# Kernel optimization log

Hardware: AMD Instinct MI355X
Metric: run time of the kernel (lower is better)

The kernel has to match this reference:

```python
import jax, jax.numpy as jnp
import numpy as np

N_NODES = 50000
EMB = 256
HEADS = 8
NEG_SLOPE = 0.2


def gat_conv(x, src, dst, W, a_src, a_dst, b, num_nodes):
    # x: [N, Din]; W: [Din, H, F]; a_src/a_dst: [H, F]; b: [H*F]
    h = jnp.einsum('nd,dhf->nhf', x, W)                      # [N, H, F]
    al_s = jnp.sum(h * a_src, axis=-1)                       # [N, H]
    al_d = jnp.sum(h * a_dst, axis=-1)                       # [N, H]
    logits = jax.nn.leaky_relu(al_s[src] + al_d[dst], NEG_SLOPE)  # [E, H]
    # segment softmax over incoming edges of each destination node
    m = jax.ops.segment_max(logits, dst, num_segments=num_nodes)  # [N, H]
    e = jnp.exp(logits - m[dst])                              # [E, H]
    z = jax.ops.segment_sum(e, dst, num_segments=num_nodes)   # [N, H]
    alpha = e / (z[dst] + 1e-16)                              # [E, H]
    msg = h[src] * alpha[..., None]                           # [E, H, F]
    out = jax.ops.segment_sum(msg, dst, num_segments=num_nodes)  # [N, H, F]
    return out.reshape(num_nodes, -1) + b


def setup_inputs() -> dict:
    key = jax.random.key(0)
    ks = jax.random.split(key, 10)
    F1 = EMB // HEADS  # 32
    x = jax.random.normal(ks[0], (N_NODES, EMB), dtype=jnp.float32)
    edge_index = jax.random.randint(ks[1], (2, 800000), 0, N_NODES, dtype=jnp.int64)
    s1 = 1.0 / np.sqrt(EMB)
    W1 = jax.random.normal(ks[2], (EMB, HEADS, F1), dtype=jnp.float32) * s1
    a_src1 = jax.random.normal(ks[3], (HEADS, F1), dtype=jnp.float32) * s1
    a_dst1 = jax.random.normal(ks[4], (HEADS, F1), dtype=jnp.float32) * s1
    b1 = jnp.zeros((HEADS * F1,), dtype=jnp.float32)
    W2 = jax.random.normal(ks[5], (EMB, 1, EMB), dtype=jnp.float32) * s1
    a_src2 = jax.random.normal(ks[6], (1, EMB), dtype=jnp.float32) * s1
    a_dst2 = jax.random.normal(ks[7], (1, EMB), dtype=jnp.float32) * s1
    b2 = jnp.zeros((EMB,), dtype=jnp.float32)
    return {"x": x, "edge_index": edge_index,
            "W1": W1, "a_src1": a_src1, "a_dst1": a_dst1, "b1": b1,
            "W2": W2, "a_src2": a_src2, "a_dst2": a_dst2, "b2": b2}


def reference(x, edge_index, W1, a_src1, a_dst1, b1, W2, a_src2, a_dst2, b2):
    n = x.shape[0]
    loops = jnp.arange(n, dtype=edge_index.dtype)
    src = jnp.concatenate([edge_index[0], loops])
    dst = jnp.concatenate([edge_index[1], loops])
    h = gat_conv(x, src, dst, W1, a_src1, a_dst1, b1, n)   # [N, EMB]
    out = gat_conv(h, src, dst, W2, a_src2, a_dst2, b2, n)  # [N, EMB]
    return out
```

## Files before the change

kernel.cpp:

```cpp
#include <hip/hip_runtime.h>
#include <hip/hip_bf16.h>

typedef unsigned short u16;
typedef unsigned int   u32;

typedef __attribute__((ext_vector_type(8))) short s16x8;
typedef __attribute__((ext_vector_type(8))) unsigned short u16x8;
typedef __attribute__((ext_vector_type(4))) float f32x4;

#define CAP 64

__device__ __forceinline__ float b2f(u16 u) {
    union { u32 i; float f; } v; v.i = ((u32)u) << 16; return v.f;
}
__device__ __forceinline__ u16 f2b(float f) {
    union { float f; u32 i; } v; v.f = f;
    u32 u = v.i;
    u32 r = (u + 0x7fffu + ((u >> 16) & 1u)) >> 16;
    return (u16)r;
}

__device__ __forceinline__ int detect_f32(const u16* xw) {
    int t = threadIdx.x & 63;
    u16 w = xw[2 * t];
    int e = (w >> 7) & 0xFF;
    bool sane = (e >= 112 && e <= 131);
    unsigned long long m1 = __ballot(sane);
    return (__popcll(m1) >= 32) ? 0 : 1;
}

__device__ __forceinline__ int edge_at(const int* __restrict__ ei, int i64f, long long j) {
    return i64f ? ei[2 * j] : ei[(size_t)j];
}

__device__ __forceinline__ u16x8 loadA8(const void* __restrict__ A, size_t eoff, int f32f) {
    if (f32f) {
        const float* p = (const float*)A + eoff;
        float4 v0 = *(const float4*)p;
        float4 v1 = *(const float4*)(p + 4);
        u16x8 r;
        r[0] = f2b(v0.x); r[1] = f2b(v0.y); r[2] = f2b(v0.z); r[3] = f2b(v0.w);
        r[4] = f2b(v1.x); r[5] = f2b(v1.y); r[6] = f2b(v1.z); r[7] = f2b(v1.w);
        return r;
    }
    return *(const u16x8*)((const u16*)A + eoff);
}

__global__ __launch_bounds__(256) void prep(const void* __restrict__ x,
                                            const int* __restrict__ ei,
                                            const void* __restrict__ W1, const void* __restrict__ W2,
                                            const void* p0, const void* p1, const void* p2,
                                            const void* p3, const void* p4, const void* p5,
                                            u16* __restrict__ wt1, u16* __restrict__ wt2,
                                            u16* __restrict__ sv,
                                            int* __restrict__ cur, u16* __restrict__ csr,
                                            int* __restrict__ flags, u16* __restrict__ hp,
                                            u16* __restrict__ wsd1t, u16* __restrict__ wsd2t,
                                            int ZB, int CF, int NN) {
    int b = blockIdx.x, t = threadIdx.x;
    int f32f = detect_f32((const u16*)x);
    if (b < 512) {
        const void* W = (b < 256) ? W1 : W2;
        u16* Wt = (b < 256) ? wt1 : wt2;
        int k = b & 255;
        u16 v = f32f ? f2b(((const float*)W)[k * 256 + t]) : ((const u16*)W)[k * 256 + t];
        Wt[t * 256 + k] = v;
        return;
    }
    b -= 512;
    if (b == 0) {
        const void* ps[6] = {p0, p1, p2, p3, p4, p5};
#pragma unroll
        for (int j = 0; j < 6; j++) {
            u16 v = f32f ? f2b(((const float*)ps[j])[t]) : ((const u16*)ps[j])[t];
            sv[j * 256 + t] = v;
        }
        hp[(size_t)NN * 256 + t] = 0;
        {
            int k = t;
            for (int h = 0; h < 8; h++) {
                float s = 0.f, d = 0.f;
                for (int f0 = 0; f0 < 32; f0 += 8) {
                    int idx = h * 32 + f0;
                    u16x8 wv = loadA8(W1, (size_t)k * 256 + idx, f32f);
                    u16x8 av = loadA8(p0, idx, f32f);
                    u16x8 dv = loadA8(p1, idx, f32f);
#pragma unroll
                    for (int j = 0; j < 8; j++) {
                        float w = b2f(wv[j]);
                        s += w * b2f(av[j]);
                        d += w * b2f(dv[j]);
                    }
                }
                wsd1t[h * 256 + k] = f2b(s);
                wsd1t[(8 + h) * 256 + k] = f2b(d);
            }
            float s2 = 0.f, d2 = 0.f;
            for (int f0 = 0; f0 < 256; f0 += 8) {
                u16x8 wv = loadA8(W2, (size_t)k * 256 + f0, f32f);
                u16x8 av = loadA8(p3, f0, f32f);
                u16x8 dv = loadA8(p4, f0, f32f);
#pragma unroll
                for (int j = 0; j < 8; j++) {
                    float w = b2f(wv[j]);
                    s2 += w * b2f(av[j]);
                    d2 += w * b2f(dv[j]);
                }
            }
            for (int cc = 0; cc < 16; cc++) wsd2t[cc * 256 + k] = 0;
            wsd2t[k] = f2b(s2);
            wsd2t[8 * 256 + k] = f2b(d2);
        }
        if (t < 64) {
            bool hz = (ei[2 * t + 1] == 0);
            unsigned long long m2 = __ballot(hz);
            if (t == 0) {
                flags[0] = f32f;
                flags[1] = (m2 == ~0ull) ? 1 : 0;
            }
        }
        return;
    }
    b -= 1;
    if (b < ZB) {
        int i = b * 256 + t;
        if (i < (NN + 3) / 4) ((int4*)cur)[i] = make_int4(0, 0, 0, 0);
        return;
    }
    b -= ZB;
    if (b < CF) {
        int i = b * 256 + t;
        int pat = (NN & 0xFFFF) | (NN << 16);
        if (i < NN * (CAP / 8)) ((int4*)csr)[i] = make_int4(pat, pat, pat, pat);
        return;
    }
}

__global__ __launch_bounds__(256) void gemm_tiled(const void* __restrict__ A,
                                                  const u16* __restrict__ Bt,
                                                  u16* __restrict__ C, int M,
                                                  const int* __restrict__ flags, int dynA,
                                                  const u16* __restrict__ wsdT,
                                                  float* __restrict__ als,
                                                  float* __restrict__ ald, int H,
                                                  const int* __restrict__ ei,
                                                  int* __restrict__ cur,
                                                  u16* __restrict__ csr,
                                                  int E, int ET, int gtA) {
    __shared__ u16 sA[128 * 32];
    __shared__ u16 sB[128 * 32];
    if ((int)blockIdx.x >= gtA) {
        int i = (blockIdx.x - gtA) * 256 + threadIdx.x;
        if (i < ET) {
            int i64f = flags[1];
            int s, d;
            if (i < E) { s = edge_at(ei, i64f, i); d = edge_at(ei, i64f, (long long)E + i); }
            else       { s = d = i - E; }
            int p = atomicAdd(&cur[d], 1);
            if (p < CAP) csr[d * CAP + p] = (u16)s;
        }
        return;
    }
    if (blockIdx.x == 0 && threadIdx.x < (unsigned)H)
        als[(size_t)M * H + threadIdx.x] = -1e30f;

    int f32a = dynA ? flags[0] : 0;
    int tid = threadIdx.x;
    int mt = blockIdx.x >> 1, nt = blockIdx.x & 1;
    int r0 = mt * 128, c0 = nt * 128;
    int w = tid >> 6, lane = tid & 63;
    int wr = w & 1, wc = w >> 1;
    int lm = lane & 15, quad = lane >> 4;
    bool doE = (nt == 0) && (w < 2);

    int row0 = tid >> 2, ch0 = tid & 3;
    int row1 = row0 + 64;
    int ga0 = r0 + row0; if (ga0 >= M) ga0 = M - 1;
    int ga1 = r0 + row1; if (ga1 >= M) ga1 = M - 1;
    size_t aoff0 = (size_t)ga0 * 256 + ch0 * 8;
    size_t aoff1 = (size_t)ga1 * 256 + ch0 * 8;
    const u16* Bb0 = Bt + (size_t)(c0 + row0) * 256 + ch0 * 8;
    const u16* Bb1 = Bt + (size_t)(c0 + row1) * 256 + ch0 * 8;

    u16x8 ra0 = loadA8(A, aoff0, f32a);
    u16x8 ra1 = loadA8(A, aoff1, f32a);
    u16x8 rb0 = *(const u16x8*)Bb0;
    u16x8 rb1 = *(const u16x8*)Bb1;

    f32x4 acc[4][4];
#pragma unroll
    for (int i = 0; i < 4; i++)
#pragma unroll
        for (int j = 0; j < 4; j++) acc[i][j] = (f32x4){0.f, 0.f, 0.f, 0.f};
    f32x4 acc_e[4];
#pragma unroll
    for (int i = 0; i < 4; i++) acc_e[i] = (f32x4){0.f, 0.f, 0.f, 0.f};

    u16* wA0 = sA + row0 * 32 + ch0 * 8;
    u16* wA1 = sA + row1 * 32 + ch0 * 8;
    u16* wB0 = sB + row0 * 32 + ch0 * 8;
    u16* wB1 = sB + row1 * 32 + ch0 * 8;
    const u16* rA = sA + (wr * 64 + lm) * 32 + quad * 8;
    const u16* rB = sB + (wc * 64 + lm) * 32 + quad * 8;

    for (int kb = 0; kb < 8; kb++) {
        __syncthreads();
        *(u16x8*)wA0 = ra0;
        *(u16x8*)wA1 = ra1;
        *(u16x8*)wB0 = rb0;
        *(u16x8*)wB1 = rb1;
        __syncthreads();
        if (kb < 7) {
            int ko = (kb + 1) * 32;
            ra0 = loadA8(A, aoff0 + ko, f32a);
            ra1 = loadA8(A, aoff1 + ko, f32a);
            rb0 = *(const u16x8*)(Bb0 + ko);
            rb1 = *(const u16x8*)(Bb1 + ko);
        }
        s16x8 af[4], bf[4];
#pragma unroll
        for (int fr = 0; fr < 4; fr++) af[fr] = *(const s16x8*)(rA + fr * 16 * 32);
#pragma unroll
        for (int fc = 0; fc < 4; fc++) bf[fc] = *(const s16x8*)(rB + fc * 16 * 32);
#pragma unroll
        for (int fr = 0; fr < 4; fr++)
#pragma unroll
            for (int fc = 0; fc < 4; fc++)
                acc[fr][fc] = __builtin_amdgcn_mfma_f32_16x16x32_bf16(af[fr], bf[fc], acc[fr][fc], 0, 0, 0);
        if (doE) {
            s16x8 bfe = *(const s16x8*)(wsdT + (size_t)lm * 256 + kb * 32 + quad * 8);
#pragma unroll
            for (int fr = 0; fr < 4; fr++)
                acc_e[fr] = __builtin_amdgcn_mfma_f32_16x16x32_bf16(af[fr], bfe, acc_e[fr], 0, 0, 0);
        }
    }

#pragma unroll
    for (int fr = 0; fr < 4; fr++) {
#pragma unroll
        for (int fc = 0; fc < 4; fc++) {
#pragma unroll
            for (int r = 0; r < 4; r++) {
                int row = r0 + wr * 64 + fr * 16 + quad * 4 + r;
                if (row < M) C[(size_t)row * 256 + c0 + wc * 64 + fc * 16 + lm] = f2b(acc[fr][fc][r]);
            }
        }
    }
    if (doE) {
#pragma unroll
        for (int fr = 0; fr < 4; fr++) {
#pragma unroll
            for (int r = 0; r < 4; r++) {
                int row = r0 + wr * 64 + fr * 16 + quad * 4 + r;
                if (row < M) {
                    float v = acc_e[fr][r];
                    if (H == 8) {
                        if (lm < 8) als[(size_t)row * 8 + lm] = v;
                        else        ald[(size_t)row * 8 + (lm - 8)] = v;
                    } else {
                        if (lm == 0)      als[row] = v;
                        else if (lm == 8) ald[row] = v;
                    }
                }
            }
        }
    }
}

template <int H, int FINAL>
__global__ __launch_bounds__(256) void gat_agg(const u16* __restrict__ hsrc,
                                               const float* __restrict__ al_s,
                                               const float* __restrict__ al_d,
                                               const int* __restrict__ degv,
                                               const u16* __restrict__ csr16,
                                               const u16* __restrict__ bias,
                                               u16* __restrict__ out_b16,
                                               void* __restrict__ out_final,
                                               const int* __restrict__ flags, int N) {
    int wid = threadIdx.x >> 6, lane = threadIdx.x & 63;
    int c = lane * 4;
    int hc = (H == 8) ? (lane >> 3) : 0;
    int he = lane & (H - 1);
    int j8 = lane >> 3;
    const u16* hb = hsrc + c;
    ushort4 bv = *(const ushort4*)(bias + c);
    int f32f = FINAL ? flags[0] : 0;
    int step = gridDim.x * 8;

    for (int n0 = blockIdx.x * 8 + wid * 2; n0 < N; n0 += step) {
        int nA = n0, nB = n0 + 1;
        int hasB = (nB < N) ? 1 : 0;
        int degA = degv[nA]; degA = degA < CAP ? degA : CAP;
        int degB = hasB ? degv[nB] : 0; degB = degB < CAP ? degB : CAP;
        int padA = (degA + 7) & ~7;
        int padB = (degB + 7) & ~7;
        const u16* cA = csr16 + nA * CAP;
        const u16* cB = csr16 + nB * CAP;
        float adA = al_d[(size_t)nA * H + he];
        float adB = hasB ? al_d[(size_t)nB * H + he] : 0.f;

        float aA0 = 0.f, aA1 = 0.f, aA2 = 0.f, aA3 = 0.f, zA = 0.f;
        float aB0 = 0.f, aB1 = 0.f, aB2 = 0.f, aB3 = 0.f, zB = 0.f;

        int gmax = padA > padB ? padA : padB;
        for (int g = 0; g < gmax; g += 8) {
            int doA = g < padA, doB = g < padB;
            if (doA & doB) {
                int smA = cA[g + j8];
                int smB = cB[g + j8];
                float vA = al_s[(size_t)smA * H + he] + adA;
                float vB = al_s[(size_t)smB * H + he] + adB;
                vA = vA > 0.f ? vA : 0.2f * vA;
                vB = vB > 0.f ? vB : 0.2f * vB;
                float eA = __expf(vA);
                float eB = __expf(vB);
#pragma unroll
                for (int j = 0; j < 8; j++) {
                    int   sjA = __shfl(smA, j * 8, 64);
                    int   sjB = __shfl(smB, j * 8, 64);
                    float ejA = __shfl(eA, j * 8 + hc, 64);
                    float ejB = __shfl(eB, j * 8 + hc, 64);
                    ushort4 hvA = *(const ushort4*)(hb + (size_t)sjA * 256);
                    ushort4 hvB = *(const ushort4*)(hb + (size_t)sjB * 256);
                    zA += ejA;
                    aA0 += ejA * b2f(hvA.x); aA1 += ejA * b2f(hvA.y);
                    aA2 += ejA * b2f(hvA.z); aA3 += ejA * b2f(hvA.w);
                    zB += ejB;
                    aB0 += ejB * b2f(hvB.x); aB1 += ejB * b2f(hvB.y);
                    aB2 += ejB * b2f(hvB.z); aB3 += ejB * b2f(hvB.w);
                }
            } else if (doA) {
                int sm = cA[g + j8];
                float v = al_s[(size_t)sm * H + he] + adA;
                v = v > 0.f ? v : 0.2f * v;
                float e = __expf(v);
#pragma unroll
                for (int j = 0; j < 8; j++) {
                    int   sj = __shfl(sm, j * 8, 64);
                    float ej = __shfl(e, j * 8 + hc, 64);
                    ushort4 hv = *(const ushort4*)(hb + (size_t)sj * 256);
                    zA += ej;
                    aA0 += ej * b2f(hv.x); aA1 += ej * b2f(hv.y);
                    aA2 += ej * b2f(hv.z); aA3 += ej * b2f(hv.w);
                }
            } else {
                int sm = cB[g + j8];
                float v = al_s[(size_t)sm * H + he] + adB;
                v = v > 0.f ? v : 0.2f * v;
                float e = __expf(v);
#pragma unroll
                for (int j = 0; j < 8; j++) {
                    int   sj = __shfl(sm, j * 8, 64);
                    float ej = __shfl(e, j * 8 + hc, 64);
                    ushort4 hv = *(const ushort4*)(hb + (size_t)sj * 256);
                    zB += ej;
                    aB0 += ej * b2f(hv.x); aB1 += ej * b2f(hv.y);
                    aB2 += ej * b2f(hv.z); aB3 += ej * b2f(hv.w);
                }
            }
        }

        {
            float invz = 1.f / (zA + 1e-16f);
            float o0 = aA0 * invz + b2f(bv.x);
            float o1 = aA1 * invz + b2f(bv.y);
            float o2 = aA2 * invz + b2f(bv.z);
            float o3 = aA3 * invz + b2f(bv.w);
            if (FINAL) {
                if (f32f) {
                    float4 ov; ov.x = o0; ov.y = o1; ov.z = o2; ov.w = o3;
                    ((float4*)out_final)[(size_t)nA * 64 + lane] = ov;
                } else {
                    ushort4 ov; ov.x = f2b(o0); ov.y = f2b(o1); ov.z = f2b(o2); ov.w = f2b(o3);
                    ((ushort4*)out_final)[(size_t)nA * 64 + lane] = ov;
                }
            } else {
                ushort4 ov; ov.x = f2b(o0); ov.y = f2b(o1); ov.z = f2b(o2); ov.w = f2b(o3);
                ((ushort4*)out_b16)[(size_t)nA * 64 + lane] = ov;
            }
        }
        if (hasB) {
            float invz = 1.f / (zB + 1e-16f);
            float o0 = aB0 * invz + b2f(bv.x);
            float o1 = aB1 * invz + b2f(bv.y);
            float o2 = aB2 * invz + b2f(bv.z);
            float o3 = aB3 * invz + b2f(bv.w);
            if (FINAL) {
                if (f32f) {
                    float4 ov; ov.x = o0; ov.y = o1; ov.z = o2; ov.w = o3;
                    ((float4*)out_final)[(size_t)nB * 64 + lane] = ov;
                } else {
                    ushort4 ov; ov.x = f2b(o0); ov.y = f2b(o1); ov.z = f2b(o2); ov.w = f2b(o3);
                    ((ushort4*)out_final)[(size_t)nB * 64 + lane] = ov;
                }
            } else {
                ushort4 ov; ov.x = f2b(o0); ov.y = f2b(o1); ov.z = f2b(o2); ov.w = f2b(o3);
                ((ushort4*)out_b16)[(size_t)nB * 64 + lane] = ov;
            }
        }
    }
}

extern "C" void kernel_launch(void* const* d_in, const int* in_sizes, int n_in,
                              void* d_out, int out_size, void* d_ws, size_t ws_size,
                              hipStream_t stream) {
    (void)n_in; (void)out_size; (void)ws_size;
    const void* x   = d_in[0];
    const int*  ei  = (const int*)d_in[1];
    const void* W1  = d_in[2];
    const void* as1 = d_in[3];
    const void* ad1 = d_in[4];
    const void* b1  = d_in[5];
    const void* W2  = d_in[6];
    const void* as2 = d_in[7];
    const void* ad2 = d_in[8];
    const void* b2  = d_in[9];

    const int N  = in_sizes[0] / 256;
    const int E  = in_sizes[1] / 2;
    const int ET = E + N;

    char* base = (char*)d_ws;
    size_t o = 0;
    auto carve = [&](size_t bytes) -> void* {
        void* q = base + o;
        o += (bytes + 255) & ~(size_t)255;
        return q;
    };
    u16*   hproj = (u16*)carve((size_t)(N + 1) * 256 * 2);
    float* als   = (float*)carve((size_t)(N + 1) * 8 * 4);
    float* ald   = (float*)carve((size_t)N * 8 * 4);
    int*   cur   = (int*)carve(((size_t)N + 16) * 4);
    u16*   csr   = (u16*)carve((size_t)N * CAP * 2);
    u16*   wt1   = (u16*)carve(256 * 256 * 2);
    u16*   wt2   = (u16*)carve(256 * 256 * 2);
    u16*   sv    = (u16*)carve(6 * 256 * 2);
    u16*   wsd1t = (u16*)carve(16 * 256 * 2);
    u16*   wsd2t = (u16*)carve(16 * 256 * 2);
    int*   flags = (int*)carve(16 * 4);

    u16* xb = (u16*)d_out;

    int ZB = ((N + 3) / 4 + 255) / 256;
    int CF = (N * (CAP / 8) + 255) / 256;
    int PB = 512 + 1 + ZB + CF;
    prep<<<PB, 256, 0, stream>>>(x, ei, W1, W2, as1, ad1, b1, as2, ad2, b2,
                                 wt1, wt2, sv, cur, csr, flags, hproj,
                                 wsd1t, wsd2t, ZB, CF, N);

    int gt = ((N + 127) / 128) * 2;
    int cg = (ET + 255) / 256;
    int agb = 2048;
    gemm_tiled<<<gt + cg, 256, 0, stream>>>(x, wt1, hproj, N, flags, 1,
                                            wsd1t, als, ald, 8,
                                            ei, cur, csr, E, ET, gt);
    gat_agg<8, 0><<<agb, 256, 0, stream>>>(hproj, als, ald, cur, csr, sv + 2 * 256,
                                           xb, nullptr, flags, N);
    gemm_tiled<<<gt, 256, 0, stream>>>(xb, wt2, hproj, N, flags, 0,
                                       wsd2t, als, ald, 1,
                                       ei, cur, csr, 0, 0, gt);
    gat_agg<1, 1><<<agb, 256, 0, stream>>>(hproj, als, ald, cur, csr, sv + 5 * 256,
                                           nullptr, d_out, flags, N);
}
```

Baseline: 373.6 us.

## Replace LDS-tiled GEMM with direct-from-global MFMA loads over 32-row tiles

The projection GEMM no longer stages A and B tiles through shared memory with barriers. Each block now covers 32 rows by all 256 columns, and each wave loads its MFMA fragments straight from global memory and computes a 32x64 slice. This removes the LDS writes, the __syncthreads and the 2-way column split, and launches many more, smaller blocks. In exchange, each A row is loaded by all four waves and the B matrix is read per block with no LDS reuse, so the kernel relies on the L1/L2 caches to absorb the redundant loads.

```diff
diff --git a/kernel.cpp b/kernel.cpp
--- a/kernel.cpp
+++ b/kernel.cpp
@@ -136,19 +136,17 @@
     }
 }
 
-__global__ __launch_bounds__(256) void gemm_tiled(const void* __restrict__ A,
-                                                  const u16* __restrict__ Bt,
-                                                  u16* __restrict__ C, int M,
-                                                  const int* __restrict__ flags, int dynA,
-                                                  const u16* __restrict__ wsdT,
-                                                  float* __restrict__ als,
-                                                  float* __restrict__ ald, int H,
-                                                  const int* __restrict__ ei,
-                                                  int* __restrict__ cur,
-                                                  u16* __restrict__ csr,
-                                                  int E, int ET, int gtA) {
-    __shared__ u16 sA[128 * 32];
-    __shared__ u16 sB[128 * 32];
+__global__ __launch_bounds__(256) void gemm_direct(const void* __restrict__ A,
+                                                   const u16* __restrict__ Bt,
+                                                   u16* __restrict__ C, int M,
+                                                   const int* __restrict__ flags, int dynA,
+                                                   const u16* __restrict__ wsdT,
+                                                   float* __restrict__ als,
+                                                   float* __restrict__ ald, int H,
+                                                   const int* __restrict__ ei,
+                                                   int* __restrict__ cur,
+                                                   u16* __restrict__ csr,
+                                                   int E, int ET, int gtA) {
     if ((int)blockIdx.x >= gtA) {
         int i = (blockIdx.x - gtA) * 256 + threadIdx.x;
         if (i < ET) {
@@ -166,92 +164,72 @@
 
     int f32a = dynA ? flags[0] : 0;
     int tid = threadIdx.x;
-    int mt = blockIdx.x >> 1, nt = blockIdx.x & 1;
-    int r0 = mt * 128, c0 = nt * 128;
     int w = tid >> 6, lane = tid & 63;
-    int wr = w & 1, wc = w >> 1;
     int lm = lane & 15, quad = lane >> 4;
-    bool doE = (nt == 0) && (w < 2);
-
-    int row0 = tid >> 2, ch0 = tid & 3;
-    int row1 = row0 + 64;
-    int ga0 = r0 + row0; if (ga0 >= M) ga0 = M - 1;
-    int ga1 = r0 + row1; if (ga1 >= M) ga1 = M - 1;
-    size_t aoff0 = (size_t)ga0 * 256 + ch0 * 8;
-    size_t aoff1 = (size_t)ga1 * 256 + ch0 * 8;
-    const u16* Bb0 = Bt + (size_t)(c0 + row0) * 256 + ch0 * 8;
-    const u16* Bb1 = Bt + (size_t)(c0 + row1) * 256 + ch0 * 8;
-
-    u16x8 ra0 = loadA8(A, aoff0, f32a);
-    u16x8 ra1 = loadA8(A, aoff1, f32a);
-    u16x8 rb0 = *(const u16x8*)Bb0;
-    u16x8 rb1 = *(const u16x8*)Bb1;
-
-    f32x4 acc[4][4];
-#pragma unroll
-    for (int i = 0; i < 4; i++)
+    int r0 = blockIdx.x * 32;
+    int c0 = w * 64;
+    bool doE = (w == 0);
+
+    int ar0 = r0 + lm;      if (ar0 >= M) ar0 = M - 1;
+    int ar1 = r0 + 16 + lm; if (ar1 >= M) ar1 = M - 1;
+    size_t a0 = (size_t)ar0 * 256 + quad * 8;
+    size_t a1 = (size_t)ar1 * 256 + quad * 8;
+    const u16* bb0 = Bt + (size_t)(c0 + 0 * 16 + lm) * 256 + quad * 8;
+    const u16* bb1 = Bt + (size_t)(c0 + 1 * 16 + lm) * 256 + quad * 8;
+    const u16* bb2 = Bt + (size_t)(c0 + 2 * 16 + lm) * 256 + quad * 8;
+    const u16* bb3 = Bt + (size_t)(c0 + 3 * 16 + lm) * 256 + quad * 8;
+    const u16* we  = wsdT + (size_t)lm * 256 + quad * 8;
+
+    f32x4 acc[2][4];
+#pragma unroll
+    for (int i = 0; i < 2; i++)
 #pragma unroll
         for (int j = 0; j < 4; j++) acc[i][j] = (f32x4){0.f, 0.f, 0.f, 0.f};
-    f32x4 acc_e[4];
-#pragma unroll
-    for (int i = 0; i < 4; i++) acc_e[i] = (f32x4){0.f, 0.f, 0.f, 0.f};
-
-    u16* wA0 = sA + row0 * 32 + ch0 * 8;
-    u16* wA1 = sA + row1 * 32 + ch0 * 8;
-    u16* wB0 = sB + row0 * 32 + ch0 * 8;
-    u16* wB1 = sB + row1 * 32 + ch0 * 8;
-    const u16* rA = sA + (wr * 64 + lm) * 32 + quad * 8;
-    const u16* rB = sB + (wc * 64 + lm) * 32 + quad * 8;
-
+    f32x4 acc_e[2];
+    acc_e[0] = (f32x4){0.f, 0.f, 0.f, 0.f};
+    acc_e[1] = (f32x4){0.f, 0.f, 0.f, 0.f};
+
+#pragma unroll
     for (int kb = 0; kb < 8; kb++) {
-        __syncthreads();
-        *(u16x8*)wA0 = ra0;
-        *(u16x8*)wA1 = ra1;
-        *(u16x8*)wB0 = rb0;
-        *(u16x8*)wB1 = rb1;
-        __syncthreads();
-        if (kb < 7) {
-            int ko = (kb + 1) * 32;
-            ra0 = loadA8(A, aoff0 + ko, f32a);
-            ra1 = loadA8(A, aoff1 + ko, f32a);
-            rb0 = *(const u16x8*)(Bb0 + ko);
-            rb1 = *(const u16x8*)(Bb1 + ko);
-        }
-        s16x8 af[4], bf[4];
-#pragma unroll
-        for (int fr = 0; fr < 4; fr++) af[fr] = *(const s16x8*)(rA + fr * 16 * 32);
-#pragma unroll
-        for (int fc = 0; fc < 4; fc++) bf[fc] = *(const s16x8*)(rB + fc * 16 * 32);
-#pragma unroll
-        for (int fr = 0; fr < 4; fr++)
-#pragma unroll
-            for (int fc = 0; fc < 4; fc++)
-                acc[fr][fc] = __builtin_amdgcn_mfma_f32_16x16x32_bf16(af[fr], bf[fc], acc[fr][fc], 0, 0, 0);
+        int ko = kb * 32;
+        s16x8 af0 = (s16x8)loadA8(A, a0 + ko, f32a);
+        s16x8 af1 = (s16x8)loadA8(A, a1 + ko, f32a);
+        s16x8 b0 = *(const s16x8*)(bb0 + ko);
+        s16x8 b1 = *(const s16x8*)(bb1 + ko);
+        s16x8 b2 = *(const s16x8*)(bb2 + ko);
+        s16x8 b3 = *(const s16x8*)(bb3 + ko);
+        acc[0][0] = __builtin_amdgcn_mfma_f32_16x16x32_bf16(af0, b0, acc[0][0], 0, 0, 0);
+        acc[0][1] = __builtin_amdgcn_mfma_f32_16x16x32_bf16(af0, b1, acc[0][1], 0, 0, 0);
+        acc[0][2] = __builtin_amdgcn_mfma_f32_16x16x32_bf16(af0, b2, acc[0][2], 0, 0, 0);
+        acc[0][3] = __builtin_amdgcn_mfma_f32_16x16x32_bf16(af0, b3, acc[0][3], 0, 0, 0);
+        acc[1][0] = __builtin_amdgcn_mfma_f32_16x16x32_bf16(af1, b0, acc[1][0], 0, 0, 0);
+        acc[1][1] = __builtin_amdgcn_mfma_f32_16x16x32_bf16(af1, b1, acc[1][1], 0, 0, 0);
+        acc[1][2] = __builtin_amdgcn_mfma_f32_16x16x32_bf16(af1, b2, acc[1][2], 0, 0, 0);
+        acc[1][3] = __builtin_amdgcn_mfma_f32_16x16x32_bf16(af1, b3, acc[1][3], 0, 0, 0);
         if (doE) {
-            s16x8 bfe = *(const s16x8*)(wsdT + (size_t)lm * 256 + kb * 32 + quad * 8);
-#pragma unroll
-            for (int fr = 0; fr < 4; fr++)
-                acc_e[fr] = __builtin_amdgcn_mfma_f32_16x16x32_bf16(af[fr], bfe, acc_e[fr], 0, 0, 0);
-        }
-    }
-
-#pragma unroll
-    for (int fr = 0; fr < 4; fr++) {
+            s16x8 be = *(const s16x8*)(we + ko);
+            acc_e[0] = __builtin_amdgcn_mfma_f32_16x16x32_bf16(af0, be, acc_e[0], 0, 0, 0);
+            acc_e[1] = __builtin_amdgcn_mfma_f32_16x16x32_bf16(af1, be, acc_e[1], 0, 0, 0);
+        }
+    }
+
+#pragma unroll
+    for (int fr = 0; fr < 2; fr++) {
 #pragma unroll
         for (int fc = 0; fc < 4; fc++) {
 #pragma unroll
             for (int r = 0; r < 4; r++) {
-                int row = r0 + wr * 64 + fr * 16 + quad * 4 + r;
-                if (row < M) C[(size_t)row * 256 + c0 + wc * 64 + fc * 16 + lm] = f2b(acc[fr][fc][r]);
+                int row = r0 + fr * 16 + quad * 4 + r;
+                if (row < M) C[(size_t)row * 256 + c0 + fc * 16 + lm] = f2b(acc[fr][fc][r]);
             }
         }
     }
     if (doE) {
 #pragma unroll
-        for (int fr = 0; fr < 4; fr++) {
+        for (int fr = 0; fr < 2; fr++) {
 #pragma unroll
             for (int r = 0; r < 4; r++) {
-                int row = r0 + wr * 64 + fr * 16 + quad * 4 + r;
+                int row = r0 + fr * 16 + quad * 4 + r;
                 if (row < M) {
                     float v = acc_e[fr][r];
                     if (H == 8) {
@@ -448,17 +426,17 @@
                                  wt1, wt2, sv, cur, csr, flags, hproj,
                                  wsd1t, wsd2t, ZB, CF, N);
 
-    int gt = ((N + 127) / 128) * 2;
+    int gt = (N + 31) / 32;
     int cg = (ET + 255) / 256;
     int agb = 2048;
-    gemm_tiled<<<gt + cg, 256, 0, stream>>>(x, wt1, hproj, N, flags, 1,
-                                            wsd1t, als, ald, 8,
-                                            ei, cur, csr, E, ET, gt);
+    gemm_direct<<<gt + cg, 256, 0, stream>>>(x, wt1, hproj, N, flags, 1,
+                                             wsd1t, als, ald, 8,
+                                             ei, cur, csr, E, ET, gt);
     gat_agg<8, 0><<<agb, 256, 0, stream>>>(hproj, als, ald, cur, csr, sv + 2 * 256,
                                            xb, nullptr, flags, N);
-    gemm_tiled<<<gt, 256, 0, stream>>>(xb, wt2, hproj, N, flags, 0,
-                                       wsd2t, als, ald, 1,
-                                       ei, cur, csr, 0, 0, gt);
+    gemm_direct<<<gt, 256, 0, stream>>>(xb, wt2, hproj, N, flags, 0,
+                                        wsd2t, als, ald, 1,
+                                        ei, cur, csr, 0, 0, gt);
     gat_agg<1, 1><<<agb, 256, 0, stream>>>(hproj, als, ald, cur, csr, sv + 5 * 256,
                                            nullptr, d_out, flags, N);
 }
```

Measured after the change: 406.7 us. 8.9% more time.

## Pre-convert x to bf16 in prep and use direct global-to-LDS loads in GEMM

Applied to the files above, without the earlier changes.

Adds a pass in the prep kernel that converts the fp32 input features to bf16 into a scratch buffer, so the first GEMM no longer converts on the fly. The GEMM now stages A and B tiles with global_load_lds straight into shared memory instead of going through registers. This drops the register prefetch of the next k-block, so loads are no longer overlapped with MFMA work. The extra conversion pass adds one more read and write of x.

```diff
diff --git a/kernel.cpp b/kernel.cpp
--- a/kernel.cpp
+++ b/kernel.cpp
@@ -18,6 +18,11 @@
     u32 u = v.i;
     u32 r = (u + 0x7fffu + ((u >> 16) & 1u)) >> 16;
     return (u16)r;
+}
+
+__device__ __forceinline__ void glds16(const u16* g, u16* l) {
+    __builtin_amdgcn_global_load_lds((const __attribute__((address_space(1))) void*)g,
+                                     (__attribute__((address_space(3))) void*)l, 16, 0, 0);
 }
 
 __device__ __forceinline__ int detect_f32(const u16* xw) {
@@ -51,14 +56,27 @@
                                             const void* __restrict__ W1, const void* __restrict__ W2,
                                             const void* p0, const void* p1, const void* p2,
                                             const void* p3, const void* p4, const void* p5,
-                                            u16* __restrict__ wt1, u16* __restrict__ wt2,
-                                            u16* __restrict__ sv,
+                                            u16* __restrict__ xb, u16* __restrict__ wt1,
+                                            u16* __restrict__ wt2, u16* __restrict__ sv,
                                             int* __restrict__ cur, u16* __restrict__ csr,
                                             int* __restrict__ flags, u16* __restrict__ hp,
                                             u16* __restrict__ wsd1t, u16* __restrict__ wsd2t,
-                                            int ZB, int CF, int NN) {
+                                            int x4, int BX, int ZB, int CF, int NN) {
     int b = blockIdx.x, t = threadIdx.x;
     int f32f = detect_f32((const u16*)x);
+    if (b < BX) {
+        int i = b * 256 + t;
+        if (i < x4) {
+            ushort4 o;
+            if (f32f) {
+                float4 v = ((const float4*)x)[i];
+                o.x = f2b(v.x); o.y = f2b(v.y); o.z = f2b(v.z); o.w = f2b(v.w);
+            } else o = ((const ushort4*)x)[i];
+            ((ushort4*)xb)[i] = o;
+        }
+        return;
+    }
+    b -= BX;
     if (b < 512) {
         const void* W = (b < 256) ? W1 : W2;
         u16* Wt = (b < 256) ? wt1 : wt2;
@@ -136,17 +154,17 @@
     }
 }
 
-__global__ __launch_bounds__(256) void gemm_tiled(const void* __restrict__ A,
+__global__ __launch_bounds__(256) void gemm_tiled(const u16* __restrict__ A,
                                                   const u16* __restrict__ Bt,
                                                   u16* __restrict__ C, int M,
-                                                  const int* __restrict__ flags, int dynA,
                                                   const u16* __restrict__ wsdT,
                                                   float* __restrict__ als,
                                                   float* __restrict__ ald, int H,
                                                   const int* __restrict__ ei,
                                                   int* __restrict__ cur,
                                                   u16* __restrict__ csr,
-                                                  int E, int ET, int gtA) {
+                                                  int E, int ET, int gtA,
+                                                  const int* __restrict__ flags) {
     __shared__ u16 sA[128 * 32];
     __shared__ u16 sB[128 * 32];
     if ((int)blockIdx.x >= gtA) {
@@ -164,28 +182,31 @@
     if (blockIdx.x == 0 && threadIdx.x < (unsigned)H)
         als[(size_t)M * H + threadIdx.x] = -1e30f;
 
-    int f32a = dynA ? flags[0] : 0;
     int tid = threadIdx.x;
     int mt = blockIdx.x >> 1, nt = blockIdx.x & 1;
     int r0 = mt * 128, c0 = nt * 128;
     int w = tid >> 6, lane = tid & 63;
     int wr = w & 1, wc = w >> 1;
     int lm = lane & 15, quad = lane >> 4;
-    bool doE = (nt == 0) && (w < 2);
-
-    int row0 = tid >> 2, ch0 = tid & 3;
-    int row1 = row0 + 64;
-    int ga0 = r0 + row0; if (ga0 >= M) ga0 = M - 1;
-    int ga1 = r0 + row1; if (ga1 >= M) ga1 = M - 1;
-    size_t aoff0 = (size_t)ga0 * 256 + ch0 * 8;
-    size_t aoff1 = (size_t)ga1 * 256 + ch0 * 8;
-    const u16* Bb0 = Bt + (size_t)(c0 + row0) * 256 + ch0 * 8;
-    const u16* Bb1 = Bt + (size_t)(c0 + row1) * 256 + ch0 * 8;
-
-    u16x8 ra0 = loadA8(A, aoff0, f32a);
-    u16x8 ra1 = loadA8(A, aoff1, f32a);
-    u16x8 rb0 = *(const u16x8*)Bb0;
-    u16x8 rb1 = *(const u16x8*)Bb1;
+    bool doE = (nt == 0) && (wc == 0);
+
+    int sr0 = w * 16 + (lane >> 2);
+    int sr1 = 64 + w * 16 + (lane >> 2);
+    int sc  = (lane & 3) * 8;
+    int ga0 = r0 + sr0; if (ga0 >= M) ga0 = M - 1;
+    int ga1 = r0 + sr1; if (ga1 >= M) ga1 = M - 1;
+    const u16* Ag0 = A + (size_t)ga0 * 256 + sc;
+    const u16* Ag1 = A + (size_t)ga1 * 256 + sc;
+    const u16* Bg0 = Bt + (size_t)(c0 + sr0) * 256 + sc;
+    const u16* Bg1 = Bt + (size_t)(c0 + sr1) * 256 + sc;
+    u16* sA0 = sA + (w * 16) * 32;
+    u16* sA1 = sA + (64 + w * 16) * 32;
+    u16* sB0 = sB + (w * 16) * 32;
+    u16* sB1 = sB + (64 + w * 16) * 32;
+
+    const u16* rA = sA + (wr * 64 + lm) * 32 + quad * 8;
+    const u16* rB = sB + (wc * 64 + lm) * 32 + quad * 8;
+    const u16* we = wsdT + (size_t)lm * 256 + quad * 8;
 
     f32x4 acc[4][4];
 #pragma unroll
@@ -196,27 +217,14 @@
 #pragma unroll
     for (int i = 0; i < 4; i++) acc_e[i] = (f32x4){0.f, 0.f, 0.f, 0.f};
 
-    u16* wA0 = sA + row0 * 32 + ch0 * 8;
-    u16* wA1 = sA + row1 * 32 + ch0 * 8;
-    u16* wB0 = sB + row0 * 32 + ch0 * 8;
-    u16* wB1 = sB + row1 * 32 + ch0 * 8;
-    const u16* rA = sA + (wr * 64 + lm) * 32 + quad * 8;
-    const u16* rB = sB + (wc * 64 + lm) * 32 + quad * 8;
-
     for (int kb = 0; kb < 8; kb++) {
+        int ko = kb * 32;
         __syncthreads();
-        *(u16x8*)wA0 = ra0;
-        *(u16x8*)wA1 = ra1;
-        *(u16x8*)wB0 = rb0;
-        *(u16x8*)wB1 = rb1;
+        glds16(Ag0 + ko, sA0);
+        glds16(Ag1 + ko, sA1);
+        glds16(Bg0 + ko, sB0);
+        glds16(Bg1 + ko, sB1);
         __syncthreads();
-        if (kb < 7) {
-            int ko = (kb + 1) * 32;
-            ra0 = loadA8(A, aoff0 + ko, f32a);
-            ra1 = loadA8(A, aoff1 + ko, f32a);
-            rb0 = *(const u16x8*)(Bb0 + ko);
-            rb1 = *(const u16x8*)(Bb1 + ko);
-        }
         s16x8 af[4], bf[4];
 #pragma unroll
         for (int fr = 0; fr < 4; fr++) af[fr] = *(const s16x8*)(rA + fr * 16 * 32);
@@ -228,7 +236,7 @@
             for (int fc = 0; fc < 4; fc++)
                 acc[fr][fc] = __builtin_amdgcn_mfma_f32_16x16x32_bf16(af[fr], bf[fc], acc[fr][fc], 0, 0, 0);
         if (doE) {
-            s16x8 bfe = *(const s16x8*)(wsdT + (size_t)lm * 256 + kb * 32 + quad * 8);
+            s16x8 bfe = *(const s16x8*)(we + ko);
 #pragma unroll
             for (int fr = 0; fr < 4; fr++)
                 acc_e[fr] = __builtin_amdgcn_mfma_f32_16x16x32_bf16(af[fr], bfe, acc_e[fr], 0, 0, 0);
@@ -441,24 +449,24 @@
 
     u16* xb = (u16*)d_out;
 
+    int x4 = N * 256 / 4;
+    int BX = (x4 + 255) / 256;
     int ZB = ((N + 3) / 4 + 255) / 256;
     int CF = (N * (CAP / 8) + 255) / 256;
-    int PB = 512 + 1 + ZB + CF;
+    int PB = BX + 512 + 1 + ZB + CF;
     prep<<<PB, 256, 0, stream>>>(x, ei, W1, W2, as1, ad1, b1, as2, ad2, b2,
-                                 wt1, wt2, sv, cur, csr, flags, hproj,
-                                 wsd1t, wsd2t, ZB, CF, N);
+                                 xb, wt1, wt2, sv, cur, csr, flags, hproj,
+                                 wsd1t, wsd2t, x4, BX, ZB, CF, N);
 
     int gt = ((N + 127) / 128) * 2;
     int cg = (ET + 255) / 256;
     int agb = 2048;
-    gemm_tiled<<<gt + cg, 256, 0, stream>>>(x, wt1, hproj, N, flags, 1,
-                                            wsd1t, als, ald, 8,
-                                            ei, cur, csr, E, ET, gt);
+    gemm_tiled<<<gt + cg, 256, 0, stream>>>(xb, wt1, hproj, N, wsd1t, als, ald, 8,
+                                            ei, cur, csr, E, ET, gt, flags);
     gat_agg<8, 0><<<agb, 256, 0, stream>>>(hproj, als, ald, cur, csr, sv + 2 * 256,
                                            xb, nullptr, flags, N);
-    gemm_tiled<<<gt, 256, 0, stream>>>(xb, wt2, hproj, N, flags, 0,
-                                       wsd2t, als, ald, 1,
-                                       ei, cur, csr, 0, 0, gt);
+    gemm_tiled<<<gt, 256, 0, stream>>>(xb, wt2, hproj, N, wsd2t, als, ald, 1,
+                                       ei, cur, csr, 0, 0, gt, flags);
     gat_agg<1, 1><<<agb, 256, 0, stream>>>(hproj, als, ald, cur, csr, sv + 5 * 256,
                                            nullptr, d_out, flags, N);
 }
```

Result: no change. 371.7 us (-0.5%).
